# Performance work log

Hardware: AMD Instinct MI355X
Metric: run time of the kernel (lower is better)

Reference implementation:

```python
import jax, jax.numpy as jnp
import numpy as np

N, F, E = 65536, 64, 16   # batch, fields, embedding_size
H1, H2 = 8, 4             # hidden_dims
BN_EPS = 1e-5


def setup_inputs() -> dict:
    key = jax.random.key(0)
    ks = jax.random.split(key, 12)
    rn = lambda k, shape, sc=1.0: jax.random.normal(k, shape, dtype=jnp.float32) * sc
    return {
        "Xa": rn(ks[0], (N, F)),
        "Xc": rn(ks[1], (N, F)),
        # per-field Linear(1,1) weights/biases (two first-order embedding lists)
        "w1": rn(ks[2], (F,)), "b1": rn(ks[3], (F,)),
        "w2": rn(ks[4], (F,)), "b2": rn(ks[5], (F,)),
        # per-field Linear(1,E) weights/biases (two second-order embedding lists)
        "W1": rn(ks[6], (F, E)), "B1": rn(ks[7], (F, E)),
        "W2": rn(ks[8], (F, E)), "B2": rn(ks[9], (F, E)),
        # deep MLP: linear_1 (F*E -> 8) + BN, linear_2 (8 -> 4). No final layer (init bug).
        "lin1_w": rn(ks[10], (H1, F * E), 0.01), "lin1_b": jnp.zeros((H1,), jnp.float32),
        "bn1_gamma": jnp.ones((H1,), jnp.float32), "bn1_beta": jnp.zeros((H1,), jnp.float32),
        "lin2_w": rn(ks[11], (H2, H1), 0.01), "lin2_b": jnp.full((H2,), 0.21, jnp.float32),
    }


def reference(Xa, Xc, w1, b1, w2, b2, W1, B1, W2, B2,
              lin1_w, lin1_b, bn1_gamma, bn1_beta, lin2_w, lin2_b):
    n = Xa.shape[0]
    # ---- FM first order (faithful to the torch broadcast: arr_2[i] is (N,N)
    # with entry [r,c] = Xa[r,i]*(w2[i]*Xc[c,i]+b2[i]); only mean over the
    # concat dim is consumed, so compute the column-mean analytically). ----
    first1 = (w1 * Xa + b1) * Xc                         # (N,F)
    xc_mean = jnp.mean(Xc, axis=0)                       # (F,)
    first2_cmean = Xa * (w2 * xc_mean + b2)              # (N,F) = mean over c of arr_2
    fm_first_mean = jnp.mean(first1 + first2_cmean, axis=1, keepdims=True)  # (N,1)

    # ---- FM second order: per-field (N,E) embeddings, fully batched. ----
    Xa3 = Xa[:, :, None]                                 # (N,F,1)
    Xc3 = Xc[:, :, None]
    emb = (Xa3 * W1 + B1) * Xc3 + Xa3 * (W2 * Xc3 + B2)  # (N,F,E)
    s = emb.sum(axis=1)                                  # (N,E)
    fm_second = 0.5 * (s * s - (emb * emb).sum(axis=1))  # (N,E)
    fm_second_mean = jnp.mean(fm_second, axis=1, keepdims=True)  # (N,1)

    # ---- deep part: cat of per-field (N,E) -> (N, F*E), field-major. ----
    deep = emb.reshape(n, F * E)
    h = deep @ lin1_w.T + lin1_b                         # (N,8)
    mu = h.mean(axis=0)
    var = h.var(axis=0)                                  # biased, as BN training mode
    h = (h - mu) / jnp.sqrt(var + BN_EPS) * bn1_gamma + bn1_beta
    h = jnp.tanh(h)                                      # dropout = identity (eval)
    h = h @ lin2_w.T + lin2_b                            # (N,4) — no final projection (init bug)
    deep_mean = h.mean(axis=1, keepdims=True)            # (N,1)

    return fm_first_mean + fm_second_mean + deep_mean    # (N,1)
```

## Files before the change

kernel.cpp:

```cpp
#include <hip/hip_runtime.h>
#include <math.h>

#define NROWS 65536
#define BN_EPS 1e-5f

#define OFF_PARTIAL 0
#define OFF_H       65536
#define OFF_REC     589824
#define OFF_BLKT    595200
#define OFF_T       693504

__global__ __launch_bounds__(256) void precompute_kernel(
    const float* __restrict__ W1, const float* __restrict__ B1,
    const float* __restrict__ W2, const float* __restrict__ B2,
    const float* __restrict__ lin1_w, const float* __restrict__ w1,
    const float* __restrict__ b1, const float* __restrict__ b2,
    float* __restrict__ rec)
{
    __shared__ float sU[1024], sB1[1024], sB2[1024];
    int tid = threadIdx.x;
    for (int i = tid; i < 1024; i += 256) {
        float u = W1[i] + W2[i];
        float x = B1[i], y = B2[i];
        sU[i] = u; sB1[i] = x; sB2[i] = y;
        int f = i >> 4, e = i & 15;
        rec[f * 84 + e]      = u;
        rec[f * 84 + 16 + e] = x;
        rec[f * 84 + 32 + e] = y;
    }
    __syncthreads();
    for (int p = tid; p < 512; p += 256) {
        int f = p >> 3, j = p & 7;
        const float* lw = lin1_w + j * 1024 + f * 16;
        float a1 = 0.f, a2 = 0.f, a3 = 0.f;
#pragma unroll
        for (int e = 0; e < 16; e++) {
            float lwv = lw[e];
            a1 = fmaf(sU[f * 16 + e], lwv, a1);
            a2 = fmaf(sB1[f * 16 + e], lwv, a2);
            a3 = fmaf(sB2[f * 16 + e], lwv, a3);
        }
        rec[f * 84 + 48 + j] = a1;
        rec[f * 84 + 56 + j] = a2;
        rec[f * 84 + 64 + j] = a3;
    }
    if (tid < 64) {
        int f = tid;
        float qu = 0.f, qb1 = 0.f, qb2 = 0.f, qub1 = 0.f, qub2 = 0.f, qb12 = 0.f;
#pragma unroll
        for (int e = 0; e < 16; e++) {
            float u = sU[f * 16 + e], x = sB1[f * 16 + e], y = sB2[f * 16 + e];
            qu   = fmaf(u, u, qu);
            qb1  = fmaf(x, x, qb1);
            qb2  = fmaf(y, y, qb2);
            qub1 = fmaf(u, x, qub1);
            qub2 = fmaf(u, y, qub2);
            qb12 = fmaf(x, y, qb12);
        }
        rec[f * 84 + 72] = qu;
        rec[f * 84 + 73] = qb1;
        rec[f * 84 + 74] = qb2;
        rec[f * 84 + 75] = 2.f * qub1;
        rec[f * 84 + 76] = 2.f * qub2;
        rec[f * 84 + 77] = 2.f * qb12;
        rec[f * 84 + 78] = w1[f];
        rec[f * 84 + 79] = b1[f];
        rec[f * 84 + 80] = b2[f];
    }
}

__global__ __launch_bounds__(256, 4) void main_kernel(
    const float* __restrict__ Xa, const float* __restrict__ Xc,
    const float* __restrict__ rec, const float* __restrict__ lin1_b,
    float* __restrict__ ws_partial, float* __restrict__ ws_h,
    float* __restrict__ ws_blkT)
{
    __shared__ float cmb[4][64][29];

    int tid  = threadIdx.x;
    int lane = tid & 63;
    int wv   = tid >> 6;
    int wu   = __builtin_amdgcn_readfirstlane(wv);
    int blk  = blockIdx.x;
    int row  = blk * 64 + lane;
    int f0   = wu * 16;

    const float4* pa = (const float4*)(Xa + (size_t)row * 64 + f0);
    const float4* pc = (const float4*)(Xc + (size_t)row * 64 + f0);
    float a_[16], c_[16];
#pragma unroll
    for (int k = 0; k < 4; k++) {
        float4 av = pa[k], cv = pc[k];
        a_[k * 4] = av.x; a_[k * 4 + 1] = av.y; a_[k * 4 + 2] = av.z; a_[k * 4 + 3] = av.w;
        c_[k * 4] = cv.x; c_[k * 4 + 1] = cv.y; c_[k * 4 + 2] = cv.z; c_[k * 4 + 3] = cv.w;
    }

    float s[16], hh[8];
#pragma unroll
    for (int e = 0; e < 16; e++) s[e] = 0.f;
#pragma unroll
    for (int j = 0; j < 8; j++) hh[j] = 0.f;
    float p1 = 0.f, p2a = 0.f, qsum = 0.f;

    const float* recw = rec + (size_t)f0 * 84;
#pragma unroll
    for (int i = 0; i < 16; i++) {
        const float* r = recw + i * 84;
        float a = a_[i], c = c_[i];
        float pp = a * c;
        p1  = fmaf(fmaf(r[78], a, r[79]), c, p1);
        p2a = fmaf(a, r[80], p2a);
        qsum = fmaf(pp * pp, r[72], qsum);
        qsum = fmaf(c * c,   r[73], qsum);
        qsum = fmaf(a * a,   r[74], qsum);
        qsum = fmaf(pp * c,  r[75], qsum);
        qsum = fmaf(pp * a,  r[76], qsum);
        qsum = fmaf(pp,      r[77], qsum);
#pragma unroll
        for (int e = 0; e < 16; e++)
            s[e] = fmaf(pp, r[e], fmaf(c, r[16 + e], fmaf(a, r[32 + e], s[e])));
#pragma unroll
        for (int j = 0; j < 8; j++)
            hh[j] = fmaf(pp, r[48 + j], fmaf(c, r[56 + j], fmaf(a, r[64 + j], hh[j])));
    }

    {
        float cs[16];
#pragma unroll
        for (int i = 0; i < 16; i++) cs[i] = c_[i];
#pragma unroll
        for (int off = 1; off < 64; off <<= 1) {
#pragma unroll
            for (int i = 0; i < 16; i++) cs[i] += __shfl_xor(cs[i], off);
        }
        if (lane == 0) {
#pragma unroll
            for (int i = 0; i < 16; i++)
                ws_blkT[(size_t)(f0 + i) * 1024 + blk] = cs[i];
        }
    }

#pragma unroll
    for (int e = 0; e < 16; e++) cmb[wv][lane][e] = s[e];
#pragma unroll
    for (int j = 0; j < 8; j++) cmb[wv][lane][16 + j] = hh[j];
    cmb[wv][lane][24] = p1;
    cmb[wv][lane][25] = p2a;
    cmb[wv][lane][26] = qsum;
    __syncthreads();

    if (tid < 64) {
        float S[16], H[8], P1 = 0.f, P2 = 0.f, Q = 0.f;
#pragma unroll
        for (int e = 0; e < 16; e++) S[e] = 0.f;
#pragma unroll
        for (int j = 0; j < 8; j++) H[j] = 0.f;
#pragma unroll
        for (int w = 0; w < 4; w++) {
#pragma unroll
            for (int e = 0; e < 16; e++) S[e] += cmb[w][tid][e];
#pragma unroll
            for (int j = 0; j < 8; j++) H[j] += cmb[w][tid][16 + j];
            P1 += cmb[w][tid][24];
            P2 += cmb[w][tid][25];
            Q  += cmb[w][tid][26];
        }
#pragma unroll
        for (int j = 0; j < 8; j++) H[j] += lin1_b[j];

        float ss = 0.f;
#pragma unroll
        for (int e = 0; e < 16; e++) ss = fmaf(S[e], S[e], ss);
        float fm2 = (ss - Q) * (0.5f / 16.f);
        int rr = blk * 64 + tid;
        ws_partial[rr] = (P1 + P2) * (1.f / 64.f) + fm2;
        *(float4*)(ws_h + (size_t)rr * 8)     = make_float4(H[0], H[1], H[2], H[3]);
        *(float4*)(ws_h + (size_t)rr * 8 + 4) = make_float4(H[4], H[5], H[6], H[7]);

        float v[16];
#pragma unroll
        for (int j = 0; j < 8; j++) { v[j] = H[j]; v[8 + j] = H[j] * H[j]; }
#pragma unroll
        for (int off = 1; off < 64; off <<= 1) {
#pragma unroll
            for (int i = 0; i < 16; i++) v[i] += __shfl_xor(v[i], off);
        }
        if (tid == 0) {
#pragma unroll
            for (int i = 0; i < 16; i++)
                ws_blkT[(size_t)(64 + i) * 1024 + blk] = v[i];
        }
    }
}

__global__ __launch_bounds__(256) void reduce_kernel(
    const float* __restrict__ ws_blkT, float* __restrict__ T)
{
    int gtid = blockIdx.x * 256 + threadIdx.x;
    int v = gtid >> 6;
    int lane = gtid & 63;
    const float* p = ws_blkT + (size_t)v * 1024 + lane;
    float acc = 0.f;
#pragma unroll
    for (int k = 0; k < 16; k++) acc += p[k * 64];
#pragma unroll
    for (int off = 32; off; off >>= 1) acc += __shfl_xor(acc, off);
    if (lane == 0) T[v] = acc;
}

__global__ __launch_bounds__(128) void final_kernel(
    const float* __restrict__ Xa, const float* __restrict__ w2,
    const float* __restrict__ gamma, const float* __restrict__ beta,
    const float* __restrict__ lin2_w, const float* __restrict__ lin2_b,
    const float* __restrict__ T, const float* __restrict__ ws_partial,
    const float* __restrict__ ws_h, float* __restrict__ out)
{
    __shared__ float sg[64], sscale[8], sshift[8], sl2w[32], sl2b[4];
    int tid = threadIdx.x;
    if (tid < 64) {
        sg[tid] = w2[tid] * (T[tid] * (1.f / 65536.f));
    } else if (tid < 72) {
        int j = tid - 64;
        float mu  = T[64 + j] * (1.f / 65536.f);
        float var = T[72 + j] * (1.f / 65536.f) - mu * mu;
        float sc = gamma[j] / sqrtf(var + BN_EPS);
        sscale[j] = sc;
        sshift[j] = beta[j] - mu * sc;
    } else if (tid < 104) {
        sl2w[tid - 72] = lin2_w[tid - 72];
    } else if (tid < 108) {
        sl2b[tid - 104] = lin2_b[tid - 104];
    }
    __syncthreads();

    int row = blockIdx.x * 128 + tid;
    const float4* xa4 = (const float4*)(Xa + (size_t)row * 64);
    float p2b = 0.f;
#pragma unroll
    for (int k = 0; k < 16; k++) {
        float4 vv = xa4[k];
        p2b += vv.x * sg[k * 4] + vv.y * sg[k * 4 + 1]
             + vv.z * sg[k * 4 + 2] + vv.w * sg[k * 4 + 3];
    }
    float4 h0 = *(const float4*)(ws_h + (size_t)row * 8);
    float4 h1 = *(const float4*)(ws_h + (size_t)row * 8 + 4);
    float hv[8] = {h0.x, h0.y, h0.z, h0.w, h1.x, h1.y, h1.z, h1.w};
    float hn[8];
#pragma unroll
    for (int j = 0; j < 8; j++)
        hn[j] = tanhf(hv[j] * sscale[j] + sshift[j]);
    float dm = 0.f;
#pragma unroll
    for (int k2 = 0; k2 < 4; k2++) {
        float o = sl2b[k2];
#pragma unroll
        for (int j = 0; j < 8; j++) o = fmaf(hn[j], sl2w[k2 * 8 + j], o);
        dm += o;
    }
    out[row] = ws_partial[row] + p2b * (1.f / 64.f) + dm * 0.25f;
}

extern "C" void kernel_launch(void* const* d_in, const int* in_sizes, int n_in,
                              void* d_out, int out_size, void* d_ws, size_t ws_size,
                              hipStream_t stream) {
    const float* Xa        = (const float*)d_in[0];
    const float* Xc        = (const float*)d_in[1];
    const float* w1        = (const float*)d_in[2];
    const float* b1        = (const float*)d_in[3];
    const float* w2        = (const float*)d_in[4];
    const float* b2        = (const float*)d_in[5];
    const float* W1        = (const float*)d_in[6];
    const float* B1        = (const float*)d_in[7];
    const float* W2        = (const float*)d_in[8];
    const float* B2        = (const float*)d_in[9];
    const float* lin1_w    = (const float*)d_in[10];
    const float* lin1_b    = (const float*)d_in[11];
    const float* bn1_gamma = (const float*)d_in[12];
    const float* bn1_beta  = (const float*)d_in[13];
    const float* lin2_w    = (const float*)d_in[14];
    const float* lin2_b    = (const float*)d_in[15];

    float* ws  = (float*)d_ws;
    float* out = (float*)d_out;

    float* ws_partial = ws + OFF_PARTIAL;
    float* ws_h       = ws + OFF_H;
    float* ws_rec     = ws + OFF_REC;
    float* ws_blkT    = ws + OFF_BLKT;
    float* ws_T       = ws + OFF_T;

    precompute_kernel<<<1, 256, 0, stream>>>(W1, B1, W2, B2, lin1_w,
                                             w1, b1, b2, ws_rec);
    main_kernel<<<1024, 256, 0, stream>>>(Xa, Xc, ws_rec, lin1_b,
                                          ws_partial, ws_h, ws_blkT);
    reduce_kernel<<<20, 256, 0, stream>>>(ws_blkT, ws_T);
    final_kernel<<<512, 128, 0, stream>>>(Xa, w2, bn1_gamma, bn1_beta,
                                          lin2_w, lin2_b, ws_T,
                                          ws_partial, ws_h, out);
}
```

Baseline: 151.4 us.

## Parallelize precompute across fields, split final rows across thread pairs, fold lin2

The precompute kernel now runs one 64-thread block per field instead of a single 256-thread block, spreading the dot products over more threads. The final kernel gives each row to two threads, each handling half the fields and half the hidden units, and combines them with a shuffle. The 4x8 lin2 matrix is folded into per-column sums, since only the mean of its outputs is used. The main kernel's occupancy hint drops from 4 to 3 waves, and the workspace offset for T moves.

```diff
diff --git a/kernel.cpp b/kernel.cpp
--- a/kernel.cpp
+++ b/kernel.cpp
@@ -8,68 +8,54 @@
 #define OFF_H       65536
 #define OFF_REC     589824
 #define OFF_BLKT    595200
-#define OFF_T       693504
-
-__global__ __launch_bounds__(256) void precompute_kernel(
+#define OFF_T       677120
+
+__global__ __launch_bounds__(64) void precompute_kernel(
     const float* __restrict__ W1, const float* __restrict__ B1,
     const float* __restrict__ W2, const float* __restrict__ B2,
     const float* __restrict__ lin1_w, const float* __restrict__ w1,
     const float* __restrict__ b1, const float* __restrict__ b2,
     float* __restrict__ rec)
 {
-    __shared__ float sU[1024], sB1[1024], sB2[1024];
-    int tid = threadIdx.x;
-    for (int i = tid; i < 1024; i += 256) {
-        float u = W1[i] + W2[i];
-        float x = B1[i], y = B2[i];
-        sU[i] = u; sB1[i] = x; sB2[i] = y;
-        int f = i >> 4, e = i & 15;
-        rec[f * 84 + e]      = u;
-        rec[f * 84 + 16 + e] = x;
-        rec[f * 84 + 32 + e] = y;
+    int f = blockIdx.x, t = threadIdx.x;
+    __shared__ float u[16], x[16], y[16];
+    if (t < 16) {
+        float uu = W1[f * 16 + t] + W2[f * 16 + t];
+        float xx = B1[f * 16 + t];
+        float yy = B2[f * 16 + t];
+        u[t] = uu; x[t] = xx; y[t] = yy;
+        rec[f * 84 + t]      = uu;
+        rec[f * 84 + 16 + t] = xx;
+        rec[f * 84 + 32 + t] = yy;
     }
     __syncthreads();
-    for (int p = tid; p < 512; p += 256) {
-        int f = p >> 3, j = p & 7;
+    if (t < 24) {
+        int j = t & 7, which = t >> 3;
+        const float* src = (which == 0) ? u : (which == 1) ? x : y;
         const float* lw = lin1_w + j * 1024 + f * 16;
-        float a1 = 0.f, a2 = 0.f, a3 = 0.f;
-#pragma unroll
-        for (int e = 0; e < 16; e++) {
-            float lwv = lw[e];
-            a1 = fmaf(sU[f * 16 + e], lwv, a1);
-            a2 = fmaf(sB1[f * 16 + e], lwv, a2);
-            a3 = fmaf(sB2[f * 16 + e], lwv, a3);
-        }
-        rec[f * 84 + 48 + j] = a1;
-        rec[f * 84 + 56 + j] = a2;
-        rec[f * 84 + 64 + j] = a3;
-    }
-    if (tid < 64) {
-        int f = tid;
-        float qu = 0.f, qb1 = 0.f, qb2 = 0.f, qub1 = 0.f, qub2 = 0.f, qb12 = 0.f;
-#pragma unroll
-        for (int e = 0; e < 16; e++) {
-            float u = sU[f * 16 + e], x = sB1[f * 16 + e], y = sB2[f * 16 + e];
-            qu   = fmaf(u, u, qu);
-            qb1  = fmaf(x, x, qb1);
-            qb2  = fmaf(y, y, qb2);
-            qub1 = fmaf(u, x, qub1);
-            qub2 = fmaf(u, y, qub2);
-            qb12 = fmaf(x, y, qb12);
-        }
-        rec[f * 84 + 72] = qu;
-        rec[f * 84 + 73] = qb1;
-        rec[f * 84 + 74] = qb2;
-        rec[f * 84 + 75] = 2.f * qub1;
-        rec[f * 84 + 76] = 2.f * qub2;
-        rec[f * 84 + 77] = 2.f * qb12;
+        float acc = 0.f;
+#pragma unroll
+        for (int e = 0; e < 16; e++) acc = fmaf(src[e], lw[e], acc);
+        rec[f * 84 + 48 + which * 8 + j] = acc;
+    } else if (t < 30) {
+        int q = t - 24;
+        const float* s1 = (q == 0 || q == 3 || q == 4) ? u : (q == 1 || q == 5) ? x : y;
+        const float* s2 = (q == 0) ? u : (q == 1 || q == 3) ? x : y;
+        float acc = 0.f;
+#pragma unroll
+        for (int e = 0; e < 16; e++) acc = fmaf(s1[e], s2[e], acc);
+        rec[f * 84 + 72 + q] = (q < 3 ? 1.f : 2.f) * acc;
+    } else if (t == 30) {
         rec[f * 84 + 78] = w1[f];
         rec[f * 84 + 79] = b1[f];
         rec[f * 84 + 80] = b2[f];
-    }
-}
-
-__global__ __launch_bounds__(256, 4) void main_kernel(
+        rec[f * 84 + 81] = 0.f;
+        rec[f * 84 + 82] = 0.f;
+        rec[f * 84 + 83] = 0.f;
+    }
+}
+
+__global__ __launch_bounds__(256, 3) void main_kernel(
     const float* __restrict__ Xa, const float* __restrict__ Xc,
     const float* __restrict__ rec, const float* __restrict__ lin1_b,
     float* __restrict__ ws_partial, float* __restrict__ ws_h,
@@ -208,14 +194,15 @@
     if (lane == 0) T[v] = acc;
 }
 
-__global__ __launch_bounds__(128) void final_kernel(
+__global__ __launch_bounds__(256) void final_kernel(
     const float* __restrict__ Xa, const float* __restrict__ w2,
     const float* __restrict__ gamma, const float* __restrict__ beta,
     const float* __restrict__ lin2_w, const float* __restrict__ lin2_b,
     const float* __restrict__ T, const float* __restrict__ ws_partial,
     const float* __restrict__ ws_h, float* __restrict__ out)
 {
-    __shared__ float sg[64], sscale[8], sshift[8], sl2w[32], sl2b[4];
+    __shared__ float sg[64], sScale[8], sShift[8], sColw[8];
+    __shared__ float sBsum;
     int tid = threadIdx.x;
     if (tid < 64) {
         sg[tid] = w2[tid] * (T[tid] * (1.f / 65536.f));
@@ -224,40 +211,43 @@
         float mu  = T[64 + j] * (1.f / 65536.f);
         float var = T[72 + j] * (1.f / 65536.f) - mu * mu;
         float sc = gamma[j] / sqrtf(var + BN_EPS);
-        sscale[j] = sc;
-        sshift[j] = beta[j] - mu * sc;
-    } else if (tid < 104) {
-        sl2w[tid - 72] = lin2_w[tid - 72];
-    } else if (tid < 108) {
-        sl2b[tid - 104] = lin2_b[tid - 104];
+        sScale[j] = sc;
+        sShift[j] = beta[j] - mu * sc;
+    } else if (tid < 80) {
+        int j = tid - 72;
+        sColw[j] = lin2_w[j] + lin2_w[8 + j] + lin2_w[16 + j] + lin2_w[24 + j];
+    } else if (tid == 80) {
+        sBsum = lin2_b[0] + lin2_b[1] + lin2_b[2] + lin2_b[3];
     }
     __syncthreads();
 
-    int row = blockIdx.x * 128 + tid;
-    const float4* xa4 = (const float4*)(Xa + (size_t)row * 64);
+    int row  = (blockIdx.x * 256 + tid) >> 1;
+    int half = tid & 1;
+    int fo   = half * 32;
+
+    const float4* xa4 = (const float4*)(Xa + (size_t)row * 64 + fo);
     float p2b = 0.f;
 #pragma unroll
-    for (int k = 0; k < 16; k++) {
+    for (int k = 0; k < 8; k++) {
         float4 vv = xa4[k];
-        p2b += vv.x * sg[k * 4] + vv.y * sg[k * 4 + 1]
-             + vv.z * sg[k * 4 + 2] + vv.w * sg[k * 4 + 3];
-    }
-    float4 h0 = *(const float4*)(ws_h + (size_t)row * 8);
-    float4 h1 = *(const float4*)(ws_h + (size_t)row * 8 + 4);
-    float hv[8] = {h0.x, h0.y, h0.z, h0.w, h1.x, h1.y, h1.z, h1.w};
-    float hn[8];
-#pragma unroll
-    for (int j = 0; j < 8; j++)
-        hn[j] = tanhf(hv[j] * sscale[j] + sshift[j]);
-    float dm = 0.f;
-#pragma unroll
-    for (int k2 = 0; k2 < 4; k2++) {
-        float o = sl2b[k2];
-#pragma unroll
-        for (int j = 0; j < 8; j++) o = fmaf(hn[j], sl2w[k2 * 8 + j], o);
-        dm += o;
-    }
-    out[row] = ws_partial[row] + p2b * (1.f / 64.f) + dm * 0.25f;
+        int b = fo + k * 4;
+        p2b += vv.x * sg[b] + vv.y * sg[b + 1] + vv.z * sg[b + 2] + vv.w * sg[b + 3];
+    }
+
+    float4 hq = *(const float4*)(ws_h + (size_t)row * 8 + half * 4);
+    float hv[4] = {hq.x, hq.y, hq.z, hq.w};
+    float dmp = 0.f;
+#pragma unroll
+    for (int jj = 0; jj < 4; jj++) {
+        int j = half * 4 + jj;
+        float hn = tanhf(hv[jj] * sScale[j] + sShift[j]);
+        dmp = fmaf(hn, sColw[j], dmp);
+    }
+
+    float val = p2b * (1.f / 64.f) + dmp * 0.25f;
+    val += __shfl_xor(val, 1);
+    if (!half)
+        out[row] = val + ws_partial[row] + sBsum * 0.25f;
 }
 
 extern "C" void kernel_launch(void* const* d_in, const int* in_sizes, int n_in,
@@ -289,12 +279,12 @@
     float* ws_blkT    = ws + OFF_BLKT;
     float* ws_T       = ws + OFF_T;
 
-    precompute_kernel<<<1, 256, 0, stream>>>(W1, B1, W2, B2, lin1_w,
+    precompute_kernel<<<64, 64, 0, stream>>>(W1, B1, W2, B2, lin1_w,
                                              w1, b1, b2, ws_rec);
     main_kernel<<<1024, 256, 0, stream>>>(Xa, Xc, ws_rec, lin1_b,
                                           ws_partial, ws_h, ws_blkT);
     reduce_kernel<<<20, 256, 0, stream>>>(ws_blkT, ws_T);
-    final_kernel<<<512, 128, 0, stream>>>(Xa, w2, bn1_gamma, bn1_beta,
+    final_kernel<<<512, 256, 0, stream>>>(Xa, w2, bn1_gamma, bn1_beta,
                                           lin2_w, lin2_b, ws_T,
                                           ws_partial, ws_h, out);
 }
```

Measured after the change: 147.3 us. -2.7%, faster.
